# Performance work log

Measured on AMD Instinct MI355X. Metric: run time of the kernel, lower is better.

## Reference

```python
import math
import jax, jax.numpy as jnp
import numpy as np

DIM = 1024
NUM_SUBKEYS = 1024
KEY_DIM = 256
CODE_DIM = 128
TOPK_SUB = 32
TOPK_FINAL = 32
B, S = 4, 2048


def setup_inputs() -> dict:
    key = jax.random.key(0)
    ks = jax.random.split(key, 7)
    x = jax.random.normal(ks[0], (B, S, DIM), dtype=jnp.float32)
    # torch Linear weight layout: (out_features, in_features)
    Wq = jax.random.normal(ks[1], (2 * KEY_DIM, DIM), dtype=jnp.float32) * (1.0 / math.sqrt(DIM))
    key_a = jax.random.normal(ks[2], (NUM_SUBKEYS, KEY_DIM), dtype=jnp.float32) * 0.02
    key_b = jax.random.normal(ks[3], (NUM_SUBKEYS, KEY_DIM), dtype=jnp.float32) * 0.02
    codes = jax.random.normal(ks[4], (NUM_SUBKEYS * NUM_SUBKEYS, CODE_DIM), dtype=jnp.float32) * 0.02
    W1 = jax.random.normal(ks[5], (DIM, CODE_DIM), dtype=jnp.float32) * (1.0 / math.sqrt(CODE_DIM))
    W2 = jax.random.normal(ks[6], (DIM, DIM), dtype=jnp.float32) * (1.0 / math.sqrt(DIM))
    return {"x": x, "Wq": Wq, "key_a": key_a, "key_b": key_b, "codes": codes, "W1": W1, "W2": W2}


def reference(x, Wq, key_a, key_b, codes, W1, W2):
    b, s, _ = x.shape
    q = (x @ Wq.T).reshape(b, s, 2, KEY_DIM)  # [B,S,2,K]
    q_a, q_b = q[:, :, 0], q[:, :, 1]
    scores_a = jnp.einsum('bsd,kd->bsk', q_a, key_a)  # [B,S,N]
    scores_b = jnp.einsum('bsd,kd->bsk', q_b, key_b)
    k_sub = min(TOPK_SUB, NUM_SUBKEYS)
    top_a_s, top_a_i = jax.lax.top_k(scores_a, k_sub)
    top_b_s, top_b_i = jax.lax.top_k(scores_b, k_sub)
    # cartesian merge: [B,S,ksub,ksub] -> [B,S,ksub*ksub]
    cand_scores = (top_a_s[..., :, None] + top_b_s[..., None, :]).reshape(b, s, -1)
    cand_indices = (top_a_i[..., :, None] * NUM_SUBKEYS + top_b_i[..., None, :]).reshape(b, s, -1)
    k_fin = min(TOPK_FINAL, cand_scores.shape[-1])
    final_scores, final_pos = jax.lax.top_k(cand_scores, k_fin)
    final_indices = jnp.take_along_axis(cand_indices, final_pos, axis=-1)  # [B,S,kf]
    sel_codes = codes[final_indices]  # gather from large table: [B,S,kf,code_dim]
    weights = jax.nn.softmax(final_scores / math.sqrt(2.0 * KEY_DIM), axis=-1)
    mixed = jnp.einsum('bsk,bskc->bsc', weights, sel_codes)  # [B,S,code_dim]
    h = jax.nn.silu(mixed @ W1.T)  # [B,S,dim]
    out = h @ W2.T
    return out
```

## Files before the change

### kernel.cpp

```cpp
#include <hip/hip_runtime.h>
#include <math.h>

#define DIM 1024
#define NSUB 1024
#define KEYD 256
#define CODED 128
#define NTOK 8192

typedef unsigned long long u64;

template<int SILU>
__global__ __launch_bounds__(256) void sgemm_nt(
    const float* __restrict__ A, const float* __restrict__ B, float* __restrict__ C,
    int M, int N, int K, int lda, int ldb, int ldc)
{
  __shared__ float As[2][8][128];
  __shared__ float Bs[2][8][128];
  const int tid = threadIdx.x;
  const int m0 = blockIdx.y * 128, n0 = blockIdx.x * 128;
  const int lrow = tid >> 1;
  const int lk   = (tid & 1) * 4;
  const int tx = tid & 15, ty = tid >> 4;
  float acc[8][8] = {{0.f}};
  const float* Ap = A + (size_t)(m0 + lrow) * lda + lk;
  const float* Bp = B + (size_t)(n0 + lrow) * ldb + lk;

  {
    float4 av = *(const float4*)(Ap);
    float4 bv = *(const float4*)(Bp);
    As[0][lk + 0][lrow] = av.x; As[0][lk + 1][lrow] = av.y;
    As[0][lk + 2][lrow] = av.z; As[0][lk + 3][lrow] = av.w;
    Bs[0][lk + 0][lrow] = bv.x; Bs[0][lk + 1][lrow] = bv.y;
    Bs[0][lk + 2][lrow] = bv.z; Bs[0][lk + 3][lrow] = bv.w;
  }
  __syncthreads();
  const int T = K >> 3;
  int cur = 0;
  for (int t = 0; t < T; ++t) {
    const int tn = (t + 1 < T) ? (t + 1) : t;
    float4 av = *(const float4*)(Ap + tn * 8);
    float4 bv = *(const float4*)(Bp + tn * 8);
#pragma unroll
    for (int k = 0; k < 8; ++k) {
      float a[8], b[8];
      *(float4*)&a[0] = *(const float4*)&As[cur][k][ty * 8];
      *(float4*)&a[4] = *(const float4*)&As[cur][k][ty * 8 + 4];
      *(float4*)&b[0] = *(const float4*)&Bs[cur][k][tx * 4];
      *(float4*)&b[4] = *(const float4*)&Bs[cur][k][64 + tx * 4];
#pragma unroll
      for (int i = 0; i < 8; ++i)
#pragma unroll
        for (int j = 0; j < 8; ++j)
          acc[i][j] = fmaf(a[i], b[j], acc[i][j]);
    }
    const int nx = cur ^ 1;
    As[nx][lk + 0][lrow] = av.x; As[nx][lk + 1][lrow] = av.y;
    As[nx][lk + 2][lrow] = av.z; As[nx][lk + 3][lrow] = av.w;
    Bs[nx][lk + 0][lrow] = bv.x; Bs[nx][lk + 1][lrow] = bv.y;
    Bs[nx][lk + 2][lrow] = bv.z; Bs[nx][lk + 3][lrow] = bv.w;
    __syncthreads();
    cur ^= 1;
  }
#pragma unroll
  for (int i = 0; i < 8; ++i) {
    float* Cp = C + (size_t)(m0 + ty * 8 + i) * ldc + n0;
    float v[8];
#pragma unroll
    for (int j = 0; j < 8; ++j) {
      float z = acc[i][j];
      if (SILU) z = z / (1.0f + expf(-z));
      v[j] = z;
    }
    *(float4*)(Cp + tx * 4)      = *(float4*)&v[0];
    *(float4*)(Cp + 64 + tx * 4) = *(float4*)&v[4];
  }
}

__device__ inline unsigned int fmap32(float f) {
  unsigned int u = __float_as_uint(f);
  return (u >> 31) ? ~u : (u | 0x80000000u);
}
__device__ inline float funmap32(unsigned int m) {
  return __uint_as_float((m & 0x80000000u) ? (m ^ 0x80000000u) : ~m);
}
__device__ inline u64 pack_key(float f, int e) {
  return ((u64)fmap32(f) << 16) | (u64)(1023 - e);
}
__device__ inline u64 shflx64(u64 v, int mask) {
  return __shfl_xor(v, mask, 64);
}
__device__ inline void cmpex(u64& x, u64 p, bool takeMax) {
  if ((x < p) == takeMax) x = p;
}

template<int NR>
__device__ inline void sort32_desc(u64* k, int l5) {
#pragma unroll 1
  for (int size = 2; size <= 32; size <<= 1) {
#pragma unroll 1
    for (int stride = size >> 1; stride > 0; stride >>= 1) {
      const bool takeMax = (((l5 & size) == 0) == ((l5 & stride) == 0));
#pragma unroll
      for (int r = 0; r < NR; ++r) {
        u64 p = shflx64(k[r], stride);
        cmpex(k[r], p, takeMax);
      }
    }
  }
}

template<int NR>
__device__ inline void bmerge32_desc(u64* k, int l5) {
#pragma unroll 1
  for (int stride = 16; stride > 0; stride >>= 1) {
    const bool takeMax = ((l5 & stride) == 0);
#pragma unroll
    for (int r = 0; r < NR; ++r) {
      u64 p = shflx64(k[r], stride);
      cmpex(k[r], p, takeMax);
    }
  }
}

template<int NR>
__device__ inline void halfmerge(u64* k, int l5) {
#pragma unroll
  for (int r = 0; r < NR; ++r) {
    u64 p = shflx64(k[r], 63);
    if (k[r] < p) k[r] = p;
  }
  bmerge32_desc<NR>(k, l5);
}

__device__ inline u64 merge2(u64 x, u64 y, int l5) {
  u64 p = shflx64(y, 31);
  if (x < p) x = p;
  bmerge32_desc<1>(&x, l5);
  return x;
}

__device__ inline u64 top32_of_1024(u64 k[16], int l5) {
  sort32_desc<16>(k, l5);
  halfmerge<16>(k, l5);
#pragma unroll
  for (int r = 0; r < 8; ++r) k[r] = merge2(k[2 * r], k[2 * r + 1], l5);
#pragma unroll
  for (int r = 0; r < 4; ++r) k[r] = merge2(k[2 * r], k[2 * r + 1], l5);
#pragma unroll
  for (int r = 0; r < 2; ++r) k[r] = merge2(k[2 * r], k[2 * r + 1], l5);
  return merge2(k[0], k[1], l5);
}

__device__ const unsigned short cand_tab[128] = {
    0,  1,  2,  3,  4,  5,  6,  7,  8,  9, 10, 11, 12, 13, 14, 15,
   16, 17, 18, 19, 20, 21, 22, 23, 24, 25, 26, 27, 28, 29, 30, 31,
   32, 33, 34, 35, 36, 37, 38, 39, 40, 41, 42, 43, 44, 45, 46, 47,
   64, 65, 66, 67, 68, 69, 70, 71, 72, 73,
   96, 97, 98, 99,100,101,102,103,
  128,129,130,131,132,133,
  160,161,162,163,164,
  192,193,194,195,
  224,225,226,227,
  256,257,258,
  288,289,290,
  320,321, 352,353, 384,385, 416,417, 448,449, 480,481,
  512,544,576,608,640,672,704,736,768,800,832,864,896,928,960,992,
  0xFFFF,0xFFFF,0xFFFF,0xFFFF,0xFFFF,0xFFFF,0xFFFF,0xFFFF,0xFFFF
};

__global__ __launch_bounds__(256) void topk_mix(
    const float* __restrict__ scores,
    const float* __restrict__ codes,
    float* __restrict__ mixed)
{
  const int lane = threadIdx.x & 63;
  const int wid  = threadIdx.x >> 6;
  const int token = blockIdx.x * 4 + wid;
  const int l5 = lane & 31;
  const float* row = scores + (size_t)token * 2048;

  u64 k[16];

#pragma unroll
  for (int r4 = 0; r4 < 4; ++r4) {
    float4 v = *(const float4*)(row + r4 * 256 + 4 * lane);
    const int e = r4 * 256 + 4 * lane;
    k[4 * r4 + 0] = pack_key(v.x, e + 0);
    k[4 * r4 + 1] = pack_key(v.y, e + 1);
    k[4 * r4 + 2] = pack_key(v.z, e + 2);
    k[4 * r4 + 3] = pack_key(v.w, e + 3);
  }
  const u64 ka = top32_of_1024(k, l5);
  const float va = funmap32((unsigned int)(ka >> 16));
  const int   ia = 1023 - (int)(ka & 0xFFFFULL);

#pragma unroll
  for (int r4 = 0; r4 < 4; ++r4) {
    float4 v = *(const float4*)(row + 1024 + r4 * 256 + 4 * lane);
    const int e = r4 * 256 + 4 * lane;
    k[4 * r4 + 0] = pack_key(v.x, e + 0);
    k[4 * r4 + 1] = pack_key(v.y, e + 1);
    k[4 * r4 + 2] = pack_key(v.z, e + 2);
    k[4 * r4 + 3] = pack_key(v.w, e + 3);
  }
  const u64 kb = top32_of_1024(k, l5);
  const float vb = funmap32((unsigned int)(kb >> 16));
  const int   ib = 1023 - (int)(kb & 0xFFFFULL);

#pragma unroll
  for (int r = 0; r < 2; ++r) {
    const int p  = cand_tab[r * 64 + lane];
    const int pi = (p == 0xFFFF) ? 0 : p;
    const float ta = __shfl(va, pi >> 5, 64);
    const float tb = __shfl(vb, pi & 31, 64);
    k[r] = (p == 0xFFFF) ? 0ULL : pack_key(ta + tb, p);
  }
  sort32_desc<2>(k, l5);
  halfmerge<2>(k, l5);
  const u64 kc = merge2(k[0], k[1], l5);
  const float cs = funmap32((unsigned int)(kc >> 16));
  const int   ps = 1023 - (int)(kc & 0xFFFFULL);
  const int cidx = __shfl(ia, ps >> 5, 64) * NSUB + __shfl(ib, ps & 31, 64);

  const float lg  = cs / 22.627416997969522f;
  const float lg0 = __shfl(lg, 0, 64);
  const float ev  = expf(lg - lg0);
  float s = ev;
#pragma unroll
  for (int m = 1; m < 32; m <<= 1) s += __shfl_xor(s, m, 64);
  const float w = ev / s;

  float2 acc = make_float2(0.f, 0.f);
#pragma unroll 8
  for (int kk = 0; kk < 32; ++kk) {
    const int   idx = __shfl(cidx, kk, 64);
    const float wk  = __shfl(w,    kk, 64);
    const float2 cv = *(const float2*)(codes + (size_t)idx * CODED + 2 * lane);
    acc.x = fmaf(wk, cv.x, acc.x);
    acc.y = fmaf(wk, cv.y, acc.y);
  }
  *(float2*)(mixed + (size_t)token * CODED + 2 * lane) = acc;
}

extern "C" void kernel_launch(void* const* d_in, const int* in_sizes, int n_in,
                              void* d_out, int out_size, void* d_ws, size_t ws_size,
                              hipStream_t stream)
{
  const float* x     = (const float*)d_in[0];
  const float* Wq    = (const float*)d_in[1];
  const float* key_a = (const float*)d_in[2];
  const float* key_b = (const float*)d_in[3];
  const float* codes = (const float*)d_in[4];
  const float* W1    = (const float*)d_in[5];
  const float* W2    = (const float*)d_in[6];
  float* out = (float*)d_out;

  char* ws = (char*)d_ws;
  float* q      = (float*)(ws);
  float* scores = (float*)(ws + (size_t)16 * 1024 * 1024);
  float* mixed  = (float*)(ws + (size_t)80 * 1024 * 1024);
  float* h      = (float*)(ws + (size_t)84 * 1024 * 1024);

  sgemm_nt<0><<<dim3(512 / 128, NTOK / 128), 256, 0, stream>>>(
      x, Wq, q, NTOK, 512, DIM, DIM, DIM, 512);
  sgemm_nt<0><<<dim3(NSUB / 128, NTOK / 128), 256, 0, stream>>>(
      q, key_a, scores, NTOK, NSUB, KEYD, 512, KEYD, 2048);
  sgemm_nt<0><<<dim3(NSUB / 128, NTOK / 128), 256, 0, stream>>>(
      q + KEYD, key_b, scores + NSUB, NTOK, NSUB, KEYD, 512, KEYD, 2048);
  topk_mix<<<NTOK / 4, 256, 0, stream>>>(scores, codes, mixed);
  sgemm_nt<1><<<dim3(DIM / 128, NTOK / 128), 256, 0, stream>>>(
      mixed, W1, h, NTOK, DIM, CODED, CODED, CODED, DIM);
  sgemm_nt<0><<<dim3(DIM / 128, NTOK / 128), 256, 0, stream>>>(
      h, W2, out, NTOK, DIM, DIM, DIM, DIM, DIM);
}
```

Measured before the change: 1.255 ms.

## Run W1/W2 GEMMs on bf16 MFMA with hi/lo split-precision emulation

Replaces the two FP32 SIMT GEMMs after the top-k mixing stage with MFMA bf16 GEMMs. Each operand is split into a high and a low bf16 part, and three MFMA products approximate FP32 accuracy. The weights are split on every call, topk_mix and the first GEMM write their outputs pre-split, and the workspace layout is reorganised to hold the new buffers. This moves the dominant W2 GEMM onto matrix cores, at the cost of extra split kernels, a small loss of accuracy, and scalar uncoalesced output stores.

```diff
diff --git a/kernel.cpp b/kernel.cpp
--- a/kernel.cpp
+++ b/kernel.cpp
@@ -8,6 +8,8 @@
 #define NTOK 8192
 
 typedef unsigned long long u64;
+typedef __attribute__((ext_vector_type(8))) short short8;
+typedef __attribute__((ext_vector_type(4))) float f32x4;
 
 template<int SILU>
 __global__ __launch_bounds__(256) void sgemm_nt(
@@ -74,6 +76,104 @@
     *(float4*)(Cp + tx * 4)      = *(float4*)&v[0];
     *(float4*)(Cp + 64 + tx * 4) = *(float4*)&v[4];
   }
+}
+
+__device__ inline unsigned bf16rne(float x) {
+  unsigned u = __float_as_uint(x);
+  return (u + 0x7FFFu + ((u >> 16) & 1u)) >> 16;
+}
+
+__global__ __launch_bounds__(256) void split_bf16(
+    const float* __restrict__ w, unsigned short* __restrict__ hi,
+    unsigned short* __restrict__ lo, int n)
+{
+  int i = blockIdx.x * 256 + threadIdx.x;
+  if (i >= n) return;
+  float x = w[i];
+  unsigned h = bf16rne(x);
+  float hf = __uint_as_float(h << 16);
+  unsigned l = bf16rne(x - hf);
+  hi[i] = (unsigned short)h;
+  lo[i] = (unsigned short)l;
+}
+
+template<int SILU, int OSPLIT>
+__global__ __launch_bounds__(256) void mgemm_nt(
+    const unsigned short* __restrict__ Ahi, const unsigned short* __restrict__ Alo,
+    const unsigned short* __restrict__ Bhi, const unsigned short* __restrict__ Blo,
+    float* __restrict__ Cf, unsigned short* __restrict__ Chi,
+    unsigned short* __restrict__ Clo, int M, int N, int K)
+{
+  __shared__ unsigned short Ah[128 * 40], Al[128 * 40], Bh[128 * 40], Bl[128 * 40];
+  const int tid = threadIdx.x;
+  const int m0 = blockIdx.y * 128, n0 = blockIdx.x * 128;
+  const int lane = tid & 63, wv = tid >> 6;
+  const int wm = (wv >> 1) * 64, wn = (wv & 1) * 64;
+  const int l15 = lane & 15, l4 = lane >> 4;
+  const int c0 = tid * 2, c1 = tid * 2 + 1;
+  const int r0 = c0 >> 2, g0 = c0 & 3, r1 = c1 >> 2, g1 = c1 & 3;
+
+  f32x4 acc[4][4];
+#pragma unroll
+  for (int i = 0; i < 4; ++i)
+#pragma unroll
+    for (int j = 0; j < 4; ++j)
+      acc[i][j] = (f32x4){0.f, 0.f, 0.f, 0.f};
+
+  for (int kt = 0; kt < K; kt += 32) {
+    __syncthreads();
+    {
+      const size_t a0 = (size_t)(m0 + r0) * K + kt + g0 * 8;
+      const size_t a1 = (size_t)(m0 + r1) * K + kt + g1 * 8;
+      const size_t b0 = (size_t)(n0 + r0) * K + kt + g0 * 8;
+      const size_t b1 = (size_t)(n0 + r1) * K + kt + g1 * 8;
+      *(uint4*)&Ah[r0 * 40 + g0 * 8] = *(const uint4*)(Ahi + a0);
+      *(uint4*)&Ah[r1 * 40 + g1 * 8] = *(const uint4*)(Ahi + a1);
+      *(uint4*)&Al[r0 * 40 + g0 * 8] = *(const uint4*)(Alo + a0);
+      *(uint4*)&Al[r1 * 40 + g1 * 8] = *(const uint4*)(Alo + a1);
+      *(uint4*)&Bh[r0 * 40 + g0 * 8] = *(const uint4*)(Bhi + b0);
+      *(uint4*)&Bh[r1 * 40 + g1 * 8] = *(const uint4*)(Bhi + b1);
+      *(uint4*)&Bl[r0 * 40 + g0 * 8] = *(const uint4*)(Blo + b0);
+      *(uint4*)&Bl[r1 * 40 + g1 * 8] = *(const uint4*)(Blo + b1);
+    }
+    __syncthreads();
+    short8 ah[4], al[4], bh[4], bl[4];
+#pragma unroll
+    for (int f = 0; f < 4; ++f) {
+      ah[f] = *(const short8*)&Ah[(wm + f * 16 + l15) * 40 + l4 * 8];
+      al[f] = *(const short8*)&Al[(wm + f * 16 + l15) * 40 + l4 * 8];
+      bh[f] = *(const short8*)&Bh[(wn + f * 16 + l15) * 40 + l4 * 8];
+      bl[f] = *(const short8*)&Bl[(wn + f * 16 + l15) * 40 + l4 * 8];
+    }
+#pragma unroll
+    for (int mf = 0; mf < 4; ++mf)
+#pragma unroll
+      for (int nf = 0; nf < 4; ++nf) {
+        acc[mf][nf] = __builtin_amdgcn_mfma_f32_16x16x32_bf16(ah[mf], bh[nf], acc[mf][nf], 0, 0, 0);
+        acc[mf][nf] = __builtin_amdgcn_mfma_f32_16x16x32_bf16(ah[mf], bl[nf], acc[mf][nf], 0, 0, 0);
+        acc[mf][nf] = __builtin_amdgcn_mfma_f32_16x16x32_bf16(al[mf], bh[nf], acc[mf][nf], 0, 0, 0);
+      }
+  }
+#pragma unroll
+  for (int mf = 0; mf < 4; ++mf)
+#pragma unroll
+    for (int nf = 0; nf < 4; ++nf)
+#pragma unroll
+      for (int j = 0; j < 4; ++j) {
+        const int gm = m0 + wm + mf * 16 + l4 * 4 + j;
+        const int gn = n0 + wn + nf * 16 + l15;
+        float z = acc[mf][nf][j];
+        if (SILU) z = z / (1.0f + expf(-z));
+        if (OSPLIT) {
+          unsigned h = bf16rne(z);
+          float hf = __uint_as_float(h << 16);
+          unsigned l = bf16rne(z - hf);
+          Chi[(size_t)gm * N + gn] = (unsigned short)h;
+          Clo[(size_t)gm * N + gn] = (unsigned short)l;
+        } else {
+          Cf[(size_t)gm * N + gn] = z;
+        }
+      }
 }
 
 __device__ inline unsigned int fmap32(float f) {
@@ -171,7 +271,8 @@
 __global__ __launch_bounds__(256) void topk_mix(
     const float* __restrict__ scores,
     const float* __restrict__ codes,
-    float* __restrict__ mixed)
+    unsigned short* __restrict__ mixedhi,
+    unsigned short* __restrict__ mixedlo)
 {
   const int lane = threadIdx.x & 63;
   const int wid  = threadIdx.x >> 6;
@@ -239,7 +340,12 @@
     acc.x = fmaf(wk, cv.x, acc.x);
     acc.y = fmaf(wk, cv.y, acc.y);
   }
-  *(float2*)(mixed + (size_t)token * CODED + 2 * lane) = acc;
+  unsigned hx = bf16rne(acc.x);
+  unsigned lx = bf16rne(acc.x - __uint_as_float(hx << 16));
+  unsigned hy = bf16rne(acc.y);
+  unsigned ly = bf16rne(acc.y - __uint_as_float(hy << 16));
+  *(unsigned*)(mixedhi + (size_t)token * CODED + 2 * lane) = hx | (hy << 16);
+  *(unsigned*)(mixedlo + (size_t)token * CODED + 2 * lane) = lx | (ly << 16);
 }
 
 extern "C" void kernel_launch(void* const* d_in, const int* in_sizes, int n_in,
@@ -257,9 +363,18 @@
 
   char* ws = (char*)d_ws;
   float* q      = (float*)(ws);
-  float* scores = (float*)(ws + (size_t)16 * 1024 * 1024);
-  float* mixed  = (float*)(ws + (size_t)80 * 1024 * 1024);
-  float* h      = (float*)(ws + (size_t)84 * 1024 * 1024);
+  float* scores = (float*)(ws + (size_t)16384 * 1024);
+  unsigned short* W1hi = (unsigned short*)(ws + (size_t)81920 * 1024);
+  unsigned short* W1lo = (unsigned short*)(ws + (size_t)82176 * 1024);
+  unsigned short* W2hi = (unsigned short*)(ws + (size_t)82432 * 1024);
+  unsigned short* W2lo = (unsigned short*)(ws + (size_t)84480 * 1024);
+  unsigned short* mixedhi = (unsigned short*)(ws + (size_t)86528 * 1024);
+  unsigned short* mixedlo = (unsigned short*)(ws + (size_t)88576 * 1024);
+  unsigned short* h_hi = (unsigned short*)(ws);
+  unsigned short* h_lo = (unsigned short*)(ws + (size_t)90624 * 1024);
+
+  split_bf16<<<DIM * CODED / 256, 256, 0, stream>>>(W1, W1hi, W1lo, DIM * CODED);
+  split_bf16<<<DIM * DIM  / 256, 256, 0, stream>>>(W2, W2hi, W2lo, DIM * DIM);
 
   sgemm_nt<0><<<dim3(512 / 128, NTOK / 128), 256, 0, stream>>>(
       x, Wq, q, NTOK, 512, DIM, DIM, DIM, 512);
@@ -267,9 +382,9 @@
       q, key_a, scores, NTOK, NSUB, KEYD, 512, KEYD, 2048);
   sgemm_nt<0><<<dim3(NSUB / 128, NTOK / 128), 256, 0, stream>>>(
       q + KEYD, key_b, scores + NSUB, NTOK, NSUB, KEYD, 512, KEYD, 2048);
-  topk_mix<<<NTOK / 4, 256, 0, stream>>>(scores, codes, mixed);
-  sgemm_nt<1><<<dim3(DIM / 128, NTOK / 128), 256, 0, stream>>>(
-      mixed, W1, h, NTOK, DIM, CODED, CODED, CODED, DIM);
-  sgemm_nt<0><<<dim3(DIM / 128, NTOK / 128), 256, 0, stream>>>(
-      h, W2, out, NTOK, DIM, DIM, DIM, DIM, DIM);
-}
+  topk_mix<<<NTOK / 4, 256, 0, stream>>>(scores, codes, mixedhi, mixedlo);
+  mgemm_nt<1, 1><<<dim3(DIM / 128, NTOK / 128), 256, 0, stream>>>(
+      mixedhi, mixedlo, W1hi, W1lo, nullptr, h_hi, h_lo, NTOK, DIM, CODED);
+  mgemm_nt<0, 0><<<dim3(DIM / 128, NTOK / 128), 256, 0, stream>>>(
+      h_hi, h_lo, W2hi, W2lo, out, nullptr, nullptr, NTOK, DIM, DIM);
+}
```

After: 1.098 ms. 12.6% less time.
